# Kernel optimization log

Measured on AMD Instinct MI355X. Metric: run time of the kernel, lower is better.

## Reference

```python
import jax, jax.numpy as jnp
import numpy as np
from functools import partial

TIMESCALES = np.array([3600.0, 14400.0, 43200.0, 172800.0, 604800.0, 2592000.0, 7776000.0, 31536000.0], dtype=np.float32)
B, T, D, H = 32, 1024, 128, 32
S = len(TIMESCALES)
LN_EPS = 1e-5


def _xavier(key, shape):
    fan_in, fan_out = shape[-1], shape[-2]
    lim = float(np.sqrt(6.0 / (fan_in + fan_out)))
    return jax.random.uniform(key, shape, jnp.float32, -lim, lim)


def setup_inputs() -> dict:
    key = jax.random.key(0)
    ks = jax.random.split(key, 12)
    x = jax.random.normal(ks[0], (B, T, D), jnp.float32)
    delta_ts = jax.random.uniform(ks[1], (B, T), jnp.float32) * 3600.0
    mask = jnp.ones((B, T, D), jnp.float32)
    # per-scale SSM cell params, stacked on leading scale axis S
    log_neg_A = jnp.log(1.0 / jnp.asarray(TIMESCALES))[:, None] * jnp.ones((S, H))  # [S,H]
    Bw = _xavier(ks[2], (S, H, D))
    Cw = _xavier(ks[3], (S, D, H))
    Dp = jnp.full((S, D), 0.1, jnp.float32)
    W1 = _xavier(ks[4], (S, H, 1 + H))
    b1 = jnp.zeros((S, H), jnp.float32)
    W2 = _xavier(ks[5], (S, 1, H))
    b2 = jnp.zeros((S, 1), jnp.float32)
    ln_g = jnp.ones((S, D), jnp.float32)
    ln_b = jnp.zeros((S, D), jnp.float32)
    # gated mixer params
    gW1 = _xavier(ks[6], (S * D, S * D))
    gb1 = jnp.zeros((S * D,), jnp.float32)
    gW2 = _xavier(ks[7], (S, S * D))
    gb2 = jnp.zeros((S,), jnp.float32)
    return dict(x=x, delta_ts=delta_ts, mask=mask, log_neg_A=log_neg_A, Bw=Bw, Cw=Cw, Dp=Dp,
                W1=W1, b1=b1, W2=W2, b2=b2, ln_g=ln_g, ln_b=ln_b,
                gW1=gW1, gb1=gb1, gW2=gW2, gb2=gb2)


def _layernorm(y, g, b):
    mu = jnp.mean(y, axis=-1, keepdims=True)
    var = jnp.mean(jnp.square(y - mu), axis=-1, keepdims=True)
    return (y - mu) * jax.lax.rsqrt(var + LN_EPS) * g + b


def _cell_scan(log_neg_A, Bw, Cw, Dp, W1, b1, W2, b2, ln_g, ln_b, x_tbd, gaps_tb1):
    """Run one SSM cell over the full sequence. x_tbd: [T,B,D], gaps: [T,B,1]."""
    A_diag = -jnp.exp(log_neg_A)  # [H]

    def step(h, inp):
        x_t, gap = inp  # [B,D], [B,1]
        z = jnp.concatenate([gap, h], axis=-1)  # [B,1+H]
        dt = jax.nn.softplus(jax.nn.silu(z @ W1.T + b1) @ W2.T + b2)  # [B,1]
        A_bar = jnp.exp(jnp.clip(A_diag[None, :] * dt, -20.0, 0.0))  # [B,H]
        h_t = jnp.clip(A_bar * h + (x_t @ Bw.T) * dt, -50.0, 50.0)
        y_t = _layernorm(h_t @ Cw.T + Dp * x_t, ln_g, ln_b)  # [B,D]
        return h_t, y_t

    h0 = jnp.zeros((x_tbd.shape[1], A_diag.shape[0]), x_tbd.dtype)
    h_final, ys = jax.lax.scan(step, h0, (x_tbd, gaps_tb1))
    return ys, h_final  # [T,B,D], [B,H]


def reference(x, delta_ts, mask, log_neg_A, Bw, Cw, Dp, W1, b1, W2, b2, ln_g, ln_b, gW1, gb1, gW2, gb2):
    xm = x * mask  # [B,T,D]
    x_tbd = jnp.transpose(xm, (1, 0, 2))  # [T,B,D]
    gaps = jnp.transpose(delta_ts)[:, :, None]  # [T,B,1]
    # vmap over the S scales (leading axis of every param)
    run = jax.vmap(_cell_scan, in_axes=(0,) * 10 + (None, None))
    ys, h_finals = run(log_neg_A, Bw, Cw, Dp, W1, b1, W2, b2, ln_g, ln_b, x_tbd, gaps)
    all_outputs = jnp.transpose(ys, (0, 2, 1, 3))  # [S,B,T,D]
    emb = all_outputs[:, :, -1, :]  # [S,B,D] last-step outputs per scale
    concat = jnp.transpose(emb, (1, 0, 2)).reshape(emb.shape[1], -1)  # [B,S*D]
    gates = jax.nn.sigmoid(jax.nn.silu(concat @ gW1.T + gb1) @ gW2.T + gb2)  # [B,S]
    mixed = jnp.einsum('sbd,bs->bd', emb, gates)  # [B,D]
    return mixed, all_outputs, h_finals
```

## Files before the change

kernel.cpp:

```cpp
#include <hip/hip_runtime.h>

#define SS 8
#define BB 32
#define TT 1024
#define DD 128
#define HH 32
#define NCHAIN (SS*BB)


__device__ __forceinline__ float expf_np(float x) {
  if (x > 88.72283935546875f) return __builtin_inff();
  if (x < -87.3365478515625f) return 0.0f;
  const float magic = 12582912.0f;
  const float q = fmaf(x, 1.44269504088896341f, magic) - magic;
  float r = fmaf(q, -6.93145752e-1f, x);
  r = fmaf(q, -1.42860677e-6f, r);
  float num = fmaf(r, 5.082762527590693718096e-04f, 6.757896990527504603057e-03f);
  num = fmaf(num, r, 5.114512081637298353406e-02f);
  num = fmaf(num, r, 2.473615434895520810817e-01f);
  num = fmaf(num, r, 7.257664613233124478488e-01f);
  num = fmaf(num, r, 9.999999999980870924916e-01f);
  float den = fmaf(r, 2.159509375685829852307e-02f, -2.742335390411667452936e-01f);
  den = fmaf(den, r, 1.0f);
  return ldexpf(num / den, (int)q);
}

__device__ __forceinline__ double exp_fast64(double x) {
  const double L2E    = 1.4426950408889634074;
  const double LN2_HI = 6.93147180369123816490e-01;
  const double LN2_LO = 1.90821492927058770002e-10;
  const double kd = rint(x * L2E);
  double t = fma(-kd, LN2_HI, x);
  t = fma(-kd, LN2_LO, t);
  const double t2 = t * t;
  const double t4 = t2 * t2;
  const double t8 = t4 * t4;
  const double qa = fma(t, 1.0 / 6.0, 0.5);
  const double qb = fma(t, 1.0 / 120.0, 1.0 / 24.0);
  const double qc = fma(t, 1.0 / 5040.0, 1.0 / 720.0);
  const double qd = fma(t, 1.0 / 362880.0, 1.0 / 40320.0);
  const double qe = fma(t, 1.0 / 39916800.0, 1.0 / 3628800.0);
  const double qf = fma(t, 1.0 / 6227020800.0, 1.0 / 479001600.0);
  const double r1 = fma(t2, qb, qa);
  const double r2 = fma(t2, qd, qc);
  const double r3 = fma(t2, qf, qe);
  double q = fma(t4, r2, r1);
  q = fma(t8, r3, q);
  const double p = fma(t2, q, 1.0 + t);
  return ldexp(p, (int)kd);
}

__device__ __forceinline__ double log1p_fast64(double y) {
  const double SQRT2M1 = 0.41421356237309504880168872420969808;
  const double ln2_hi  = 6.93147180369123816490e-01;
  const double ln2_lo  = 1.90821492927058770002e-10;
  const double Lp1 = 6.666666666666735130e-01;
  const double Lp2 = 3.999999999940941908e-01;
  const double Lp3 = 2.857142874366239149e-01;
  const double Lp4 = 2.222219843214978396e-01;
  const double Lp5 = 1.818357216161805012e-01;
  const double Lp6 = 1.531383769920937332e-01;
  const double Lp7 = 1.479819860511658591e-01;
  const bool big = (y > SQRT2M1);
  const double kd = big ? 1.0 : 0.0;
  const double f  = big ? (y - 1.0) * 0.5 : y;
  const double d  = 2.0 + f;
  double rr = (double)__builtin_amdgcn_rcpf((float)d);
  rr = fma(fma(-d, rr, 1.0), rr, rr);
  rr = fma(fma(-d, rr, 1.0), rr, rr);
  const double s  = f * rr;
  const double z  = s * s;
  const double z2 = z * z;
  const double z4 = z2 * z2;
  const double A1 = fma(z, Lp2, Lp1);
  const double A2 = fma(z, Lp4, Lp3);
  const double A3 = fma(z, Lp6, Lp5);
  const double B1 = fma(z2, A2, A1);
  const double B2 = fma(z2, Lp7, A3);
  const double P  = fma(z4, B2, B1);
  const double R  = z * P;
  const double hfsq = 0.5 * f * f;
  return kd * ln2_hi - ((hfsq - (s * (hfsq + R) + kd * ln2_lo)) - f);
}

__device__ __forceinline__ float expf_cr(float x)   { return (float)exp_fast64((double)x); }
__device__ __forceinline__ float log1pf_cr(float x) { return (float)log1p_fast64((double)x); }

__device__ __forceinline__ float red32_add(float x) {
  int xi;
  xi = __builtin_amdgcn_update_dpp(0, __float_as_int(x), 0xB1, 0xF, 0xF, true);
  x += __int_as_float(xi);
  xi = __builtin_amdgcn_update_dpp(0, __float_as_int(x), 0x4E, 0xF, 0xF, true);
  x += __int_as_float(xi);
  xi = __builtin_amdgcn_update_dpp(0, __float_as_int(x), 0x141, 0xF, 0xF, true);
  x += __int_as_float(xi);
  xi = __builtin_amdgcn_update_dpp(0, __float_as_int(x), 0x140, 0xF, 0xF, true);
  x += __int_as_float(xi);
  x += __int_as_float(__builtin_amdgcn_ds_swizzle(__float_as_int(x), 0x401F));
  return x;
}

#define SWZ(x, pat) __int_as_float(__builtin_amdgcn_ds_swizzle(__float_as_int(x), (pat)))
#define DPPF(x, ctrl) __int_as_float(__builtin_amdgcn_update_dpp(0, __float_as_int(x), (ctrl), 0xF, 0xF, true))

#if __has_builtin(__builtin_amdgcn_permlane16_swap)
__device__ __forceinline__ float xor16_lane(float u) {
  const unsigned ub = (unsigned)__float_as_int(u);
  auto pr = __builtin_amdgcn_permlane16_swap(ub, ub, false, false);
  return __int_as_float((int)(pr[0] ^ pr[1] ^ ub));
}
#else
__device__ __forceinline__ float xor16_lane(float u) {
  return SWZ(u, 0x401F);
}
#endif

__global__ __launch_bounds__(256) void k_xb(const float* __restrict__ x,
                                            const float* __restrict__ mask,
                                            const float* __restrict__ Bw,
                                            float* __restrict__ xb) {
  __shared__ float bw_sh[HH][132];
  __shared__ float x_sh[8][132];
  const int r0 = blockIdx.x * 8;
  const int chain = r0 >> 10;
  const int s = chain >> 5;
  const int b = chain & 31;
  const int tid = threadIdx.x;
  for (int i = tid; i < HH * DD; i += 256)
    bw_sh[i >> 7][i & 127] = Bw[s * HH * DD + i];
  const int t0 = r0 & 1023;
  for (int i = tid; i < 8 * DD; i += 256) {
    int rr = i >> 7, d = i & 127;
    size_t gidx = ((size_t)b * TT + t0 + rr) * DD + d;
    x_sh[rr][d] = x[gidx] * mask[gidx];
  }
  __syncthreads();
  const int rl = tid >> 5;
  const int j  = tid & 31;
  float a = 0.0f;
  for (int d = 0; d < DD; ++d)
    a = fmaf(x_sh[rl][d], bw_sh[j][d], a);
  xb[(size_t)(r0 + rl) * DD + j] = a;
}

#define SCAN_STEP(GAPC, XOWNC, GAPN, XOWNN, TCUR, TNXT)                          \
  {                                                                              \
    GAPN  = dts[(TNXT)];                                                         \
    XOWNN = xrow[(size_t)(TNXT) * DD + j];                                       \
    float a = fmaf(w1f[0], (GAPC), 0.0f);                                        \
    _Pragma("unroll")                                                            \
    for (int k = 0; k < HH; ++k) {                                               \
      const float hk = __int_as_float(                                           \
          __builtin_amdgcn_readlane(__float_as_int(h_own), k));                  \
      a = fmaf(w1f[1 + k], hk, a);                                               \
    }                                                                            \
    a = a + b1j;                                                                 \
    const float sg = 1.0f / (1.0f + expf_np(-a));                                \
    const float u = a * sg;                                                      \
    const float u16 = xor16_lane(u);              \
    const float u8  = DPPF(u, 0x128);             \
    const float u24 = DPPF(u16, 0x128);           \
    float acc = fmaf(u,   w2a, 0.0f);                                            \
    acc = fmaf(u8,  w2b, acc);                                                   \
    acc = fmaf(u16, w2c, acc);                                                   \
    acc = fmaf(u24, w2d, acc);                                                   \
    const float acc4 = DPPF(acc, 0x104);               \
    const float tf   = __fadd_rn(acc, acc4);                                     \
    const float p01  = __fadd_rn(tf, DPPF(tf, 0xB1));                            \
    const float rs   = __fadd_rn(p01, DPPF(p01, 0x4E));                          \
    float r = __int_as_float(__builtin_amdgcn_readfirstlane(__float_as_int(rs)));\
    r = r + b2s;                                                                 \
    const float dt0 = fmaxf(r, 0.0f) + log1pf_cr(expf_cr(-fabsf(r)));            \
    float ad = adj * dt0;                                                        \
    ad = fminf(fmaxf(ad, -20.0f), 0.0f);                                         \
    const float ab = expf_np(ad);                                                \
    {                                                                            \
      const float p1 = __fmul_rn(ab, h_own);                                     \
      const float p2 = __fmul_rn((XOWNC), dt0);                                  \
      float hk2 = __fadd_rn(p1, p2);                                             \
      hk2 = fminf(fmaxf(hk2, -50.0f), 50.0f);                                    \
      h_own = hk2;                                                               \
    }                                                                            \
    hsp[(size_t)(TCUR) * DD] = h_own;                                            \
  }

__global__ __launch_bounds__(64) void k_scan(const float* __restrict__ xb,
                                             float* __restrict__ out_f,
                                             const float* __restrict__ delta_ts,
                                             const float* __restrict__ log_neg_A,
                                             const float* __restrict__ W1,
                                             const float* __restrict__ b1,
                                             const float* __restrict__ W2,
                                             const float* __restrict__ b2,
                                             float* __restrict__ hfin) {
  const int j = threadIdx.x;
  const int chain = blockIdx.x;
  const int s = chain >> 5, b = chain & 31;

  float w1f[33];
  #pragma unroll
  for (int k = 0; k < 33; ++k) w1f[k] = W1[(s * HH + j) * 33 + k];
  const float b1j = b1[s * HH + j];
  const float b2s = b2[s];
  const float adj = -expf_np(log_neg_A[s * HH + j]);
  const float w2a = W2[s * HH + j];
  const float w2b = W2[s * HH + (j ^ 8)];
  const float w2c = W2[s * HH + (j ^ 16)];
  const float w2d = W2[s * HH + (j ^ 24)];

  const float* xrow = xb + (size_t)chain * TT * DD;
  const float* dts  = delta_ts + b * TT;
  float* hsp = out_f + 4096 + (size_t)chain * TT * DD + 96 + j;

  float h_own = 0.0f;

  float gapA  = dts[0], gapB;
  float xownA = xrow[j], xownB;

  #pragma unroll 1
  for (int t = 0; t < TT; t += 2) {
    SCAN_STEP(gapA, xownA, gapB, xownB, t, t + 1)
    SCAN_STEP(gapB, xownB, gapA, xownA, t + 1, (t + 2) & 1023)
  }
  hfin[chain * HH + j] = h_own;
}

__global__ __launch_bounds__(256) void k_out(float* __restrict__ out_f,
                                             const float* __restrict__ x,
                                             const float* __restrict__ mask,
                                             const float* __restrict__ Cw,
                                             const float* __restrict__ Dp,
                                             const float* __restrict__ ln_g,
                                             const float* __restrict__ ln_b) {
  __shared__ float cw_sh[HH][132];
  __shared__ float h_sh[2][8][32];
  float* all_out = out_f + 4096;
  const int tid = threadIdx.x;
  const int half = blockIdx.x & 1;
  const int chain = blockIdx.x >> 1;
  const int s = chain >> 5, b = chain & 31;
  for (int i = tid; i < DD * HH; i += 256) {
    int d = i >> 5, k = i & 31;
    cw_sh[k][d] = Cw[((size_t)s * DD + d) * HH + k];
  }
  const int grp = tid >> 5;
  const int l = tid & 31;
  const int d0 = l * 4;
  const float4 dp4 = *(const float4*)&Dp[s * DD + d0];
  const float4 g4  = *(const float4*)&ln_g[s * DD + d0];
  const float4 be4 = *(const float4*)&ln_b[s * DD + d0];
  __syncthreads();
  for (int it = 0; it < 64; ++it) {
    const int buf = it & 1;
    const int tbase = half * 512 + it * 8;
    {
      int rr = tid >> 5, k = tid & 31;
      h_sh[buf][rr][k] = all_out[((size_t)chain * TT + tbase + rr) * DD + 96 + k];
    }
    __syncthreads();
    const int t = tbase + grp;
    const size_t xoff = ((size_t)b * TT + t) * DD + d0;
    float4 xv = *(const float4*)&x[xoff];
    float4 mv = *(const float4*)&mask[xoff];
    float4 v;
    v.x = dp4.x * xv.x * mv.x;
    v.y = dp4.y * xv.y * mv.y;
    v.z = dp4.z * xv.z * mv.z;
    v.w = dp4.w * xv.w * mv.w;
    const float4* hv = (const float4*)&h_sh[buf][grp][0];
    #pragma unroll
    for (int q = 0; q < 8; ++q) {
      float4 hq = hv[q];
      float hc[4] = {hq.x, hq.y, hq.z, hq.w};
      #pragma unroll
      for (int c = 0; c < 4; ++c) {
        float4 cw = *(const float4*)&cw_sh[4 * q + c][d0];
        float hk = hc[c];
        v.x = fmaf(hk, cw.x, v.x);
        v.y = fmaf(hk, cw.y, v.y);
        v.z = fmaf(hk, cw.z, v.z);
        v.w = fmaf(hk, cw.w, v.w);
      }
    }
    float sum = red32_add((v.x + v.y) + (v.z + v.w));
    float mu = sum * (1.0f / 128.0f);
    float dx = v.x - mu, dy = v.y - mu, dz = v.z - mu, dw = v.w - mu;
    float ss = red32_add((dx * dx + dy * dy) + (dz * dz + dw * dw));
    float var = ss * (1.0f / 128.0f);
    float sc = rsqrtf(var + 1e-5f);
    float4 o;
    o.x = fmaf(dx * sc, g4.x, be4.x);
    o.y = fmaf(dy * sc, g4.y, be4.y);
    o.z = fmaf(dz * sc, g4.z, be4.z);
    o.w = fmaf(dw * sc, g4.w, be4.w);
    *(float4*)&all_out[((size_t)chain * TT + t) * DD + d0] = o;
  }
}

__global__ __launch_bounds__(256) void k_g1(const float* __restrict__ all_out,
                                            const float* __restrict__ gW1,
                                            const float* __restrict__ gb1,
                                            float* __restrict__ g1) {
  const int idx = blockIdx.x * 256 + threadIdx.x;
  const int b = idx & 31, i = idx >> 5;
  const float* wrow = gW1 + (size_t)i * 1024;
  float a0 = 0.f, a1 = 0.f, a2 = 0.f, a3 = 0.f;
  for (int j4 = 0; j4 < 1024; j4 += 4) {
    float4 w = *(const float4*)&wrow[j4];
    int sI = j4 >> 7, d = j4 & 127;
    float4 c = *(const float4*)&all_out[(((size_t)(sI * 32 + b)) * TT + 1023) * DD + d];
    a0 = fmaf(w.x, c.x, a0);
    a1 = fmaf(w.y, c.y, a1);
    a2 = fmaf(w.z, c.z, a2);
    a3 = fmaf(w.w, c.w, a3);
  }
  float r = (a0 + a1) + (a2 + a3) + gb1[i];
  g1[b * 1024 + i] = r * (1.0f / (1.0f + expf(-r)));
}

__global__ __launch_bounds__(256) void k_gate(const float* __restrict__ g1,
                                              const float* __restrict__ gW2,
                                              const float* __restrict__ gb2,
                                              const float* __restrict__ all_out,
                                              float* __restrict__ mixed) {
  __shared__ float gates_sh[32][8];
  const int tid = threadIdx.x;
  const int b = tid & 31, s2 = tid >> 5;
  const float* grow = g1 + b * 1024;
  const float* wrow = gW2 + s2 * 1024;
  float a0 = 0.f, a1 = 0.f, a2 = 0.f, a3 = 0.f;
  for (int i = 0; i < 1024; i += 4) {
    float4 gg = *(const float4*)&grow[i];
    float4 w  = *(const float4*)&wrow[i];
    a0 = fmaf(gg.x, w.x, a0);
    a1 = fmaf(gg.y, w.y, a1);
    a2 = fmaf(gg.z, w.z, a2);
    a3 = fmaf(gg.w, w.w, a3);
  }
  float r = (a0 + a1) + (a2 + a3) + gb2[s2];
  gates_sh[b][s2] = 1.0f / (1.0f + expf(-r));
  __syncthreads();
  for (int m = tid; m < BB * DD; m += 256) {
    int bb = m >> 7, d = m & 127;
    float acc = 0.f;
    #pragma unroll
    for (int ss2 = 0; ss2 < 8; ++ss2)
      acc = fmaf(all_out[(((size_t)(ss2 * 32 + bb)) * TT + 1023) * DD + d],
                 gates_sh[bb][ss2], acc);
    mixed[m] = acc;
  }
}

extern "C" void kernel_launch(void* const* d_in, const int* in_sizes, int n_in,
                              void* d_out, int out_size, void* d_ws, size_t ws_size,
                              hipStream_t stream) {
  const float* x         = (const float*)d_in[0];
  const float* delta_ts  = (const float*)d_in[1];
  const float* mask      = (const float*)d_in[2];
  const float* log_neg_A = (const float*)d_in[3];
  const float* Bw        = (const float*)d_in[4];
  const float* Cw        = (const float*)d_in[5];
  const float* Dp        = (const float*)d_in[6];
  const float* W1        = (const float*)d_in[7];
  const float* b1        = (const float*)d_in[8];
  const float* W2        = (const float*)d_in[9];
  const float* b2        = (const float*)d_in[10];
  const float* ln_g      = (const float*)d_in[11];
  const float* ln_b      = (const float*)d_in[12];
  const float* gW1       = (const float*)d_in[13];
  const float* gb1       = (const float*)d_in[14];
  const float* gW2       = (const float*)d_in[15];
  const float* gb2       = (const float*)d_in[16];

  float*  out_f   = (float*)d_out;
  float*  mixed   = out_f;
  float*  all_out = out_f + 4096;
  float*  hfin    = out_f + 4096 + (size_t)SS * BB * TT * DD;
  float*  xb      = out_f + 4096;

  float* g1 = (float*)d_ws;

  k_xb  <<<NCHAIN * TT / 8, 256, 0, stream>>>(x, mask, Bw, xb);
  k_scan<<<NCHAIN, 32, 0, stream>>>(xb, out_f, delta_ts, log_neg_A, W1, b1, W2, b2, hfin);
  k_out <<<NCHAIN * 2, 256, 0, stream>>>(out_f, x, mask, Cw, Dp, ln_g, ln_b);
  k_g1  <<<BB * 1024 / 256, 256, 0, stream>>>(all_out, gW1, gb1, g1);
  k_gate<<<1, 256, 0, stream>>>(g1, gW2, gb2, all_out, mixed);
}
```

Before: 1.081 ms.

## Fuse x·Bw projection into scan kernel, computing next step inside recurrence

Removes the separate k_xb kernel that wrote the projected input to global memory. The scan kernel now loads x and mask for step t+2 and computes the x·Bw projection for the next step with readlane broadcasts. Bw rows are kept in registers, and the projection is issued off the h-dependent critical path so it can overlap the recurrence. This saves a kernel launch and a round trip of the intermediate through memory, at the cost of about 128 extra multiply-adds and readlanes per step on a serial 256-wave scan, plus heavy register pressure.

```diff
diff --git a/kernel.cpp b/kernel.cpp
--- a/kernel.cpp
+++ b/kernel.cpp
@@ -103,6 +103,10 @@
 #define SWZ(x, pat) __int_as_float(__builtin_amdgcn_ds_swizzle(__float_as_int(x), (pat)))
 #define DPPF(x, ctrl) __int_as_float(__builtin_amdgcn_update_dpp(0, __float_as_int(x), (ctrl), 0xF, 0xF, true))
 
+__device__ __forceinline__ float rl_f(float v, int l) {
+  return __int_as_float(__builtin_amdgcn_readlane(__float_as_int(v), l));
+}
+
 #if __has_builtin(__builtin_amdgcn_permlane16_swap)
 __device__ __forceinline__ float xor16_lane(float u) {
   const unsigned ub = (unsigned)__float_as_int(u);
@@ -115,43 +119,31 @@
 }
 #endif
 
-__global__ __launch_bounds__(256) void k_xb(const float* __restrict__ x,
-                                            const float* __restrict__ mask,
-                                            const float* __restrict__ Bw,
-                                            float* __restrict__ xb) {
-  __shared__ float bw_sh[HH][132];
-  __shared__ float x_sh[8][132];
-  const int r0 = blockIdx.x * 8;
-  const int chain = r0 >> 10;
-  const int s = chain >> 5;
-  const int b = chain & 31;
-  const int tid = threadIdx.x;
-  for (int i = tid; i < HH * DD; i += 256)
-    bw_sh[i >> 7][i & 127] = Bw[s * HH * DD + i];
-  const int t0 = r0 & 1023;
-  for (int i = tid; i < 8 * DD; i += 256) {
-    int rr = i >> 7, d = i & 127;
-    size_t gidx = ((size_t)b * TT + t0 + rr) * DD + d;
-    x_sh[rr][d] = x[gidx] * mask[gidx];
-  }
-  __syncthreads();
-  const int rl = tid >> 5;
-  const int j  = tid & 31;
-  float a = 0.0f;
-  for (int d = 0; d < DD; ++d)
-    a = fmaf(x_sh[rl][d], bw_sh[j][d], a);
-  xb[(size_t)(r0 + rl) * DD + j] = a;
-}
-
-#define SCAN_STEP(GAPC, XOWNC, GAPN, XOWNN, TCUR, TNXT)                          \
+#define SCAN_STEP(GAPC, GAPN, XLC, MLC, XLN, MLN, TCUR)                          \
   {                                                                              \
-    GAPN  = dts[(TNXT)];                                                         \
-    XOWNN = xrow[(size_t)(TNXT) * DD + j];                                       \
+    const int tld_ = ((TCUR) + 2) & 1023;                                        \
+    XLN = *(const float4*)(xg + (size_t)tld_ * DD + 4 * j);                      \
+    MLN = *(const float4*)(mg + (size_t)tld_ * DD + 4 * j);                      \
+    GAPN = dts[((TCUR) + 1) & 1023];                                             \
+                      \
+    const float xm0_ = __fmul_rn(XLC.x, MLC.x);                                  \
+    const float xm1_ = __fmul_rn(XLC.y, MLC.y);                                  \
+    const float xm2_ = __fmul_rn(XLC.z, MLC.z);                                  \
+    const float xm3_ = __fmul_rn(XLC.w, MLC.w);                                  \
+            \
+    float xbN_ = 0.0f;                                                           \
+    _Pragma("unroll")                                                            \
+    for (int l = 0; l < 32; ++l) {                                               \
+      xbN_ = fmaf(rl_f(xm0_, l), bw[4 * l + 0], xbN_);                           \
+      xbN_ = fmaf(rl_f(xm1_, l), bw[4 * l + 1], xbN_);                           \
+      xbN_ = fmaf(rl_f(xm2_, l), bw[4 * l + 2], xbN_);                           \
+      xbN_ = fmaf(rl_f(xm3_, l), bw[4 * l + 3], xbN_);                           \
+    }                                                                            \
+                             \
     float a = fmaf(w1f[0], (GAPC), 0.0f);                                        \
     _Pragma("unroll")                                                            \
     for (int k = 0; k < HH; ++k) {                                               \
-      const float hk = __int_as_float(                                           \
-          __builtin_amdgcn_readlane(__float_as_int(h_own), k));                  \
+      const float hk = rl_f(h_own, k);                                           \
       a = fmaf(w1f[1 + k], hk, a);                                               \
     }                                                                            \
     a = a + b1j;                                                                 \
@@ -176,15 +168,18 @@
     const float ab = expf_np(ad);                                                \
     {                                                                            \
       const float p1 = __fmul_rn(ab, h_own);                                     \
-      const float p2 = __fmul_rn((XOWNC), dt0);                                  \
+      const float p2 = __fmul_rn(xbA, dt0);                                      \
       float hk2 = __fadd_rn(p1, p2);                                             \
       hk2 = fminf(fmaxf(hk2, -50.0f), 50.0f);                                    \
       h_own = hk2;                                                               \
     }                                                                            \
     hsp[(size_t)(TCUR) * DD] = h_own;                                            \
-  }
-
-__global__ __launch_bounds__(64) void k_scan(const float* __restrict__ xb,
+    xbA = xbN_;                                                                  \
+  }
+
+__global__ __launch_bounds__(64) void k_scan(const float* __restrict__ x,
+                                             const float* __restrict__ mask,
+                                             const float* __restrict__ Bw,
                                              float* __restrict__ out_f,
                                              const float* __restrict__ delta_ts,
                                              const float* __restrict__ log_neg_A,
@@ -208,19 +203,51 @@
   const float w2c = W2[s * HH + (j ^ 16)];
   const float w2d = W2[s * HH + (j ^ 24)];
 
-  const float* xrow = xb + (size_t)chain * TT * DD;
-  const float* dts  = delta_ts + b * TT;
+  float bw[DD];
+  {
+    const float* bwp = Bw + ((size_t)s * HH + j) * DD;
+    #pragma unroll
+    for (int d4 = 0; d4 < DD; d4 += 4) {
+      const float4 t4 = *(const float4*)(bwp + d4);
+      bw[d4 + 0] = t4.x; bw[d4 + 1] = t4.y;
+      bw[d4 + 2] = t4.z; bw[d4 + 3] = t4.w;
+    }
+  }
+
+  const float* xg  = x    + (size_t)b * TT * DD;
+  const float* mg  = mask + (size_t)b * TT * DD;
+  const float* dts = delta_ts + b * TT;
   float* hsp = out_f + 4096 + (size_t)chain * TT * DD + 96 + j;
 
   float h_own = 0.0f;
 
-  float gapA  = dts[0], gapB;
-  float xownA = xrow[j], xownB;
+  float xbA;
+  {
+    const float4 x0 = *(const float4*)(xg + 4 * j);
+    const float4 m0 = *(const float4*)(mg + 4 * j);
+    const float a0 = __fmul_rn(x0.x, m0.x);
+    const float a1 = __fmul_rn(x0.y, m0.y);
+    const float a2 = __fmul_rn(x0.z, m0.z);
+    const float a3 = __fmul_rn(x0.w, m0.w);
+    float acc0 = 0.0f;
+    #pragma unroll
+    for (int l = 0; l < 32; ++l) {
+      acc0 = fmaf(rl_f(a0, l), bw[4 * l + 0], acc0);
+      acc0 = fmaf(rl_f(a1, l), bw[4 * l + 1], acc0);
+      acc0 = fmaf(rl_f(a2, l), bw[4 * l + 2], acc0);
+      acc0 = fmaf(rl_f(a3, l), bw[4 * l + 3], acc0);
+    }
+    xbA = acc0;
+  }
+  float4 xLa = *(const float4*)(xg + DD + 4 * j);
+  float4 mLa = *(const float4*)(mg + DD + 4 * j);
+  float4 xLb, mLb;
+  float gapA = dts[0], gapB;
 
   #pragma unroll 1
   for (int t = 0; t < TT; t += 2) {
-    SCAN_STEP(gapA, xownA, gapB, xownB, t, t + 1)
-    SCAN_STEP(gapB, xownB, gapA, xownA, t + 1, (t + 2) & 1023)
+    SCAN_STEP(gapA, gapB, xLa, mLa, xLb, mLb, t)
+    SCAN_STEP(gapB, gapA, xLb, mLb, xLa, mLa, t + 1)
   }
   hfin[chain * HH + j] = h_own;
 }
@@ -376,12 +403,10 @@
   float*  mixed   = out_f;
   float*  all_out = out_f + 4096;
   float*  hfin    = out_f + 4096 + (size_t)SS * BB * TT * DD;
-  float*  xb      = out_f + 4096;
 
   float* g1 = (float*)d_ws;
 
-  k_xb  <<<NCHAIN * TT / 8, 256, 0, stream>>>(x, mask, Bw, xb);
-  k_scan<<<NCHAIN, 32, 0, stream>>>(xb, out_f, delta_ts, log_neg_A, W1, b1, W2, b2, hfin);
+  k_scan<<<NCHAIN, 32, 0, stream>>>(x, mask, Bw, out_f, delta_ts, log_neg_A, W1, b1, W2, b2, hfin);
   k_out <<<NCHAIN * 2, 256, 0, stream>>>(out_f, x, mask, Cw, Dp, ln_g, ln_b);
   k_g1  <<<BB * 1024 / 256, 256, 0, stream>>>(all_out, gW1, gb1, g1);
   k_gate<<<1, 256, 0, stream>>>(g1, gW2, gb2, all_out, mixed);
```

After: 2.732 ms. 153% more time.
